# Performance work log

Measured on AMD Instinct MI355X. Metric: run time of the kernel, lower is better.

The kernel has to match this reference:

```python
import jax, jax.numpy as jnp
import numpy as np

B, S, I, H = 2, 400, 80, 128
F = 2 * H            # bidirectional feature dim
N = S + 1            # zero row prepended -> pairwise grid size
MAX_SEG = 50
NCLS = 50


def prelu(x, a):
    return jnp.where(x >= 0, x, a * x)


def lstm_dir(x, Wi, Wh, b, reverse=False):
    # x: (B, S, I); torch gate order: i, f, g, o
    if reverse:
        x = x[:, ::-1]
    Hd = Wh.shape[1]

    def step(carry, xt):
        h, c = carry
        gates = xt @ Wi.T + h @ Wh.T + b
        i_, f_, g_, o_ = jnp.split(gates, 4, axis=-1)
        c = jax.nn.sigmoid(f_) * c + jax.nn.sigmoid(i_) * jnp.tanh(g_)
        h = jax.nn.sigmoid(o_) * jnp.tanh(c)
        return (h, c), h

    h0 = jnp.zeros((x.shape[0], Hd), x.dtype)
    _, hs = jax.lax.scan(step, (h0, h0), jnp.swapaxes(x, 0, 1))
    hs = jnp.swapaxes(hs, 0, 1)
    if reverse:
        hs = hs[:, ::-1]
    return hs


def setup_inputs() -> dict:
    key = jax.random.key(0)
    ks = jax.random.split(key, 16)

    def rn(k, shape, s=0.05):
        return jax.random.normal(k, shape, jnp.float32) * s

    inp = {
        "x": jax.random.normal(ks[0], (B, S, I), jnp.float32),
        "lengths": jnp.full((B,), S, jnp.int32),
        "Wi_f": rn(ks[1], (4 * H, I)), "Wh_f": rn(ks[2], (4 * H, H)), "b_f": jnp.zeros((4 * H,), jnp.float32),
        "Wi_b": rn(ks[3], (4 * H, I)), "Wh_b": rn(ks[4], (4 * H, H)), "b_b": jnp.zeros((4 * H,), jnp.float32),
        "a1": jnp.full((1,), 0.25, jnp.float32),
        "W1": rn(ks[5], (100, 3 * F)), "b1": jnp.zeros((100,), jnp.float32),
        "a2": jnp.full((1,), 0.25, jnp.float32),
        "W2": rn(ks[6], (1, 100)), "b2": jnp.zeros((1,), jnp.float32),
        "ac1": jnp.full((1,), 0.25, jnp.float32),
        "Wc1": rn(ks[7], (2 * NCLS, F)), "bc1": jnp.zeros((2 * NCLS,), jnp.float32),
        "ac2": jnp.full((1,), 0.25, jnp.float32),
        "Wc2": rn(ks[8], (NCLS, 2 * NCLS)), "bc2": jnp.zeros((NCLS,), jnp.float32),
        "ab1": jnp.full((1,), 0.25, jnp.float32),
        "Wb1": rn(ks[9], (2 * NCLS, F)), "bb1": jnp.zeros((2 * NCLS,), jnp.float32),
        "ab2": jnp.full((1,), 0.25, jnp.float32),
        "Wb2": rn(ks[10], (2, 2 * NCLS)), "bb2": jnp.zeros((2,), jnp.float32),
    }
    return inp


def compute_scores(x, Wi_f, Wh_f, b_f, Wi_b, Wh_b, b_b, a1, W1, b1, a2, W2, b2):
    rnn_out = jnp.concatenate(
        [lstm_dir(x, Wi_f, Wh_f, b_f, False), lstm_dir(x, Wi_b, Wh_b, b_b, True)], axis=-1
    )  # (B, S, F)
    xp = jnp.concatenate([jnp.zeros((x.shape[0], 1, F), x.dtype), rnn_out], axis=1)  # (B, N, F)
    cum = jnp.cumsum(xp, axis=1)
    # phi[b,i,j] = concat(cum[j]-cum[i], xp[i], xp[j]); PReLU is elementwise with a
    # single shared parameter, and the first Linear is additive across the concat
    # blocks, so we decompose W1 instead of materializing the (B,N,N,3F) tensor.
    W1c, W1d, W1e = W1[:, :F], W1[:, F:2 * F], W1[:, 2 * F:]
    pc = prelu(cum[:, None, :, :] - cum[:, :, None, :], a1)  # (B, N, N, F)
    pxd = prelu(xp, a1) @ W1d.T                              # (B, N, 100)
    pxe = prelu(xp, a1) @ W1e.T                              # (B, N, 100)
    h = jnp.einsum('bijf,kf->bijk', pc, W1c) + pxd[:, :, None, :] + pxe[:, None, :, :] + b1
    scores = (prelu(h, a2) @ W2.T + b2)[..., 0]              # (B, N, N)
    return rnn_out, scores


def segment_search(scores):
    # DP: best[i] = max_{max(0,i-MAX_SEG) <= k < i} best[k] + scores[:, k, i]
    Bn, Nn = scores.shape[0], scores.shape[1]
    ks = jnp.arange(Nn)

    def dp_step(best, i):
        col = jnp.take(scores, i, axis=2)                    # (B, N)
        mask = (ks >= i - MAX_SEG) & (ks < i)
        cand = jnp.where(mask[None, :], best + col, -jnp.inf)
        m = cand.max(axis=1)
        k = cand.argmax(axis=1)
        best = best.at[:, i].set(m)
        return best, k

    best0 = jnp.zeros((Bn, Nn), scores.dtype)
    best, prev_tail = jax.lax.scan(dp_step, best0, jnp.arange(1, Nn))
    prev = jnp.concatenate([jnp.zeros((Bn, 1), jnp.int32),
                            prev_tail.T.astype(jnp.int32)], axis=1)  # (B, N)
    return best, prev


def reference(x, lengths, Wi_f, Wh_f, b_f, Wi_b, Wh_b, b_b, a1, W1, b1, a2, W2, b2,
              ac1, Wc1, bc1, ac2, Wc2, bc2, ab1, Wb1, bb1, ab2, Wb2, bb2):
    rnn_out, scores = compute_scores(x, Wi_f, Wh_f, b_f, Wi_b, Wh_b, b_b,
                                     a1, W1, b1, a2, W2, b2)
    cls_out = prelu(prelu(rnn_out, ac1) @ Wc1.T + bc1, ac2) @ Wc2.T + bc2
    bin_out = prelu(prelu(rnn_out, ab1) @ Wb1.T + bb1, ab2) @ Wb2.T + bb2
    best, prev = segment_search(scores)
    # pred score for the best segmentation ending at `lengths[b]` equals best[b, L]
    pred_scores = best[jnp.arange(scores.shape[0]), lengths]
    return scores, cls_out, bin_out, pred_scores, prev
```

## Files before the change

### kernel.cpp

```cpp
#include <hip/hip_runtime.h>
#include <hip/hip_fp16.h>
#include <math.h>

#define BB 2
#define SS 400
#define II 80
#define HH 128
#define FF 256
#define NN 401
#define G4 512
#define MAXSEG 50
#define NCLS 50
#define KH 100
#define KP 112
#define FRAGF 14336

#define SCORES_OFF 0
#define CLS_OFF    (BB*NN*NN)
#define BIN_OFF    (CLS_OFF + BB*SS*NCLS)
#define PRED_OFF   (BIN_OFF + BB*SS*2)
#define PREV_OFF   (PRED_OFF + BB)

#define WS_GX      0
#define WS_RNN     (WS_GX + 4*SS*G4)
#define WS_CUM     (WS_RNN + BB*SS*FF)
#define WS_PXD     (WS_CUM + BB*NN*FF)
#define WS_PXE     (WS_PXD + BB*NN*KP)
#define WS_PART    (WS_PXE + BB*NN*KP)
#define WS_W2P     (WS_PART + BB*16*FF)
#define WS_B1P     (WS_W2P + KP)
#define WS_WHP     (WS_B1P + KP)
#define WS_WFRAGC  (WS_WHP + 65536)
#define WS_WFRAGD  (WS_WFRAGC + FRAGF)
#define WS_WFRAGE  (WS_WFRAGD + FRAGF)
#define WS_WFRAGHC (WS_WFRAGE + FRAGF)
#define WS_WFRAGHB (WS_WFRAGHC + FRAGF)
#define WS_BC1P    (WS_WFRAGHB + FRAGF)
#define WS_BB1P    (WS_BC1P + KP)

typedef __attribute__((ext_vector_type(8))) short short8;
typedef __attribute__((ext_vector_type(4))) float f32x4;
typedef _Float16 f16x2 __attribute__((ext_vector_type(2)));
typedef _Float16 f16x8 __attribute__((ext_vector_type(8)));

__device__ __forceinline__ float prelu_f(float x, float a) {
    return x >= 0.f ? x : a * x;
}
__device__ __forceinline__ unsigned short f2bf(float x) {
    union { float f; unsigned u; } v; v.f = x;
    unsigned r = v.u + 0x7fffu + ((v.u >> 16) & 1u);
    return (unsigned short)(r >> 16);
}
__device__ __forceinline__ float fast_sigmoid(float x) {
    return 1.f / (1.f + __expf(-x));
}
__device__ __forceinline__ float fast_tanh(float x) {
    return 1.f - 2.f / (1.f + __expf(2.f * x));
}
__device__ __forceinline__ void barrier_lds() {
    asm volatile("s_waitcnt lgkmcnt(0)\ns_barrier" ::: "memory");
}
__device__ __forceinline__ void rec_barrier() {
    __builtin_amdgcn_sched_barrier(0);
    asm volatile("s_waitcnt lgkmcnt(0)");
    __builtin_amdgcn_s_barrier();
    __builtin_amdgcn_sched_barrier(0);
}
__device__ __forceinline__ int fragidx(int k, int f) {
    int kt = k >> 4, l15 = k & 15;
    int ks = f >> 5, quad = (f >> 3) & 3, e = f & 7;
    return ((((kt * 8 + ks) * 4 + quad) * 16) + l15) * 8 + e;
}

#define WPACKS (5 * KP)
#define PREPBLKS (WPACKS + G4)
__global__ void k_lstm_pre(const float* __restrict__ x,
                           const float* __restrict__ Wi_f, const float* __restrict__ b_f,
                           const float* __restrict__ Wi_b, const float* __restrict__ b_b,
                           float* __restrict__ gx,
                           const float* __restrict__ W1, const float* __restrict__ W2,
                           const float* __restrict__ b1,
                           const float* __restrict__ Wh_f, const float* __restrict__ Wh_b,
                           const float* __restrict__ Wc1, const float* __restrict__ Wb1,
                           const float* __restrict__ bc1, const float* __restrict__ bb1,
                           short* __restrict__ wfC, short* __restrict__ wfD,
                           short* __restrict__ wfE, short* __restrict__ wfHC,
                           short* __restrict__ wfHB,
                           float* __restrict__ w2p, float* __restrict__ b1p,
                           float* __restrict__ bc1p, float* __restrict__ bb1p,
                           __half* __restrict__ whp) {
    int blk0 = blockIdx.x;
    int tid = threadIdx.x;
    if (blk0 < WPACKS) {
        int which = blk0 / KP;
        int k = blk0 % KP;
        float w = 0.f;
        short* dst = wfC;
        if (which == 0)      { if (k < KH) w = W1[k * (3 * FF) + tid];          dst = wfC; }
        else if (which == 1) { if (k < KH) w = W1[k * (3 * FF) + FF + tid];     dst = wfD; }
        else if (which == 2) { if (k < KH) w = W1[k * (3 * FF) + 2 * FF + tid]; dst = wfE; }
        else if (which == 3) { if (k < KH) w = Wc1[k * FF + tid];               dst = wfHC; }
        else                 { if (k < KH) w = Wb1[k * FF + tid];               dst = wfHB; }
        dst[fragidx(k, tid)] = (short)f2bf(w);
        if (tid == 0) {
            if (which == 0) {
                w2p[k] = (k < KH) ? W2[k] : 0.f;
                b1p[k] = (k < KH) ? b1[k] : 0.f;
            } else if (which == 3) {
                bc1p[k] = (k < KH) ? bc1[k] : 0.f;
            } else if (which == 4) {
                bb1p[k] = (k < KH) ? bb1[k] : 0.f;
            }
        }
        return;
    }
    if (blk0 < PREPBLKS) {
        int gq = blk0 - WPACKS;
        int gate = gq >> 7;
        int unit = gq & 127;
        int wv = unit >> 4, col = unit & 15;
        int dir = tid >> 7, k = tid & 127;
        int kt = k >> 5, lanehi = (k >> 3) & 3, e = k & 7;
        int lane = lanehi * 16 + col;
        const float* Wh = dir ? Wh_b : Wh_f;
        whp[(size_t)(((((dir * 4 + gate) * 8 + wv) * 4 + kt) * 64) + lane) * 8 + e] =
            (__half)Wh[gq * HH + k];
        return;
    }
    int blk = blk0 - PREPBLKS;
    int t = blk % SS;
    int db = blk / SS;
    int b = db & 1, dir = db >> 1;
    const float* Wi = dir ? Wi_b : Wi_f;
    const float* bias = dir ? b_b : b_f;
    int xt = dir ? (SS - 1 - t) : t;

    __shared__ __align__(16) float xr[II];
    if (tid < II) xr[tid] = x[(b * SS + xt) * II + tid];
    __syncthreads();

    for (int g = tid; g < G4; g += 256) {
        const float* w = Wi + g * II;
        float acc = bias[g];
#pragma unroll
        for (int i = 0; i < II; i += 4) {
            float4 w4 = *(const float4*)(w + i);
            acc += w4.x * xr[i] + w4.y * xr[i + 1] + w4.z * xr[i + 2] + w4.w * xr[i + 3];
        }
        gx[((size_t)(db * SS + t) * HH + (g & 127)) * 4 + (g >> 7)] = acc;
    }
}

__global__ __launch_bounds__(512, 1)
void k_lstm_rec(const _Float16* __restrict__ whf, const float* __restrict__ gxr,
                float* __restrict__ rnn_out) {
    int db = blockIdx.x;
    int b = db & 1, dir = db >> 1;
    int tid = threadIdx.x;
    int wv = tid >> 6;
    int lane = tid & 63;

    f16x8 bf[4][4];
    {
        const f16x8* wp = (const f16x8*)whf;
#pragma unroll
        for (int g = 0; g < 4; ++g)
#pragma unroll
            for (int kt = 0; kt < 4; ++kt)
                bf[g][kt] = wp[((((dir * 4 + g) * 8 + wv) * 4 + kt) * 64) + lane];
    }

    __shared__ __align__(16) __half hsf[2][128];
    for (int i = tid; i < 256; i += 512) (&hsf[0][0])[i] = (__half)0.f;
    __syncthreads();

    float c_state = 0.f;
    const float4* gp4 = (const float4*)gxr + (size_t)(db * SS) * HH
                      + (wv << 4) + (lane & 15);

    float4 g0 = make_float4(0,0,0,0), g1 = g0, g2 = g0, g3 = g0;
    if (lane < 16) {
        g0 = gp4[0 * HH];
        g1 = gp4[1 * HH];
        g2 = gp4[2 * HH];
        g3 = gp4[3 * HH];
    }
    const float4* gq = gp4 + (size_t)4 * HH;

    float* outp = rnn_out + ((size_t)b * SS + (dir ? (SS - 1) : 0)) * FF
                + dir * HH + (wv << 4) + lane;
    const int ostep = dir ? -FF : FF;

    const f32x4 z4 = (f32x4){0.f, 0.f, 0.f, 0.f};
    int pb = 0;
    int hib = (lane >> 4) * 8;

#define REC_STEP(G, PF) do {                                                   \
        f16x8 a0 = *(const f16x8*)(&hsf[pb][ 0 + hib]);                        \
        f16x8 a1 = *(const f16x8*)(&hsf[pb][32 + hib]);                        \
        f16x8 a2 = *(const f16x8*)(&hsf[pb][64 + hib]);                        \
        f16x8 a3 = *(const f16x8*)(&hsf[pb][96 + hib]);                        \
        f32x4 acc0 = __builtin_amdgcn_mfma_f32_16x16x32_f16(a0, bf[0][0], z4, 0, 0, 0); \
        f32x4 acc1 = __builtin_amdgcn_mfma_f32_16x16x32_f16(a0, bf[1][0], z4, 0, 0, 0); \
        f32x4 acc2 = __builtin_amdgcn_mfma_f32_16x16x32_f16(a0, bf[2][0], z4, 0, 0, 0); \
        f32x4 acc3 = __builtin_amdgcn_mfma_f32_16x16x32_f16(a0, bf[3][0], z4, 0, 0, 0); \
        acc0 = __builtin_amdgcn_mfma_f32_16x16x32_f16(a1, bf[0][1], acc0, 0, 0, 0); \
        acc1 = __builtin_amdgcn_mfma_f32_16x16x32_f16(a1, bf[1][1], acc1, 0, 0, 0); \
        acc2 = __builtin_amdgcn_mfma_f32_16x16x32_f16(a1, bf[2][1], acc2, 0, 0, 0); \
        acc3 = __builtin_amdgcn_mfma_f32_16x16x32_f16(a1, bf[3][1], acc3, 0, 0, 0); \
        acc0 = __builtin_amdgcn_mfma_f32_16x16x32_f16(a2, bf[0][2], acc0, 0, 0, 0); \
        acc1 = __builtin_amdgcn_mfma_f32_16x16x32_f16(a2, bf[1][2], acc1, 0, 0, 0); \
        acc2 = __builtin_amdgcn_mfma_f32_16x16x32_f16(a2, bf[2][2], acc2, 0, 0, 0); \
        acc3 = __builtin_amdgcn_mfma_f32_16x16x32_f16(a2, bf[3][2], acc3, 0, 0, 0); \
        acc0 = __builtin_amdgcn_mfma_f32_16x16x32_f16(a3, bf[0][3], acc0, 0, 0, 0); \
        acc1 = __builtin_amdgcn_mfma_f32_16x16x32_f16(a3, bf[1][3], acc1, 0, 0, 0); \
        acc2 = __builtin_amdgcn_mfma_f32_16x16x32_f16(a3, bf[2][3], acc2, 0, 0, 0); \
        acc3 = __builtin_amdgcn_mfma_f32_16x16x32_f16(a3, bf[3][3], acc3, 0, 0, 0); \
        if (lane < 16) {                                                       \
            float gi = acc0[0] + G.x;                                          \
            float gf = acc1[0] + G.y;                                          \
            float gg = acc2[0] + G.z;                                          \
            float go = acc3[0] + G.w;                                          \
            if (PF) { G = *gq; gq += HH; }         \
            c_state = fast_sigmoid(gf) * c_state + fast_sigmoid(gi) * fast_tanh(gg); \
            float h = fast_sigmoid(go) * fast_tanh(c_state);                   \
            hsf[pb ^ 1][(wv << 4) + lane] = (__half)h;                         \
            *outp = h;                                                         \
            outp += ostep;                                                     \
        }                                                                      \
        rec_barrier();                                                         \
        pb ^= 1;                                                               \
    } while (0)

    for (int it = 0; it < 99; ++it) {
        REC_STEP(g0, 1);
        REC_STEP(g1, 1);
        REC_STEP(g2, 1);
        REC_STEP(g3, 1);
    }
    REC_STEP(g0, 0);
    REC_STEP(g1, 0);
    REC_STEP(g2, 0);
    REC_STEP(g3, 0);
#undef REC_STEP
}

__global__ void k_cum(const float* __restrict__ rnn, float* __restrict__ cum) {
    int b = blockIdx.x;
    int f = threadIdx.x;
    float run = 0.f;
    cum[(size_t)(b * NN) * FF + f] = 0.f;
    const float* rp = rnn + (size_t)b * SS * FF + f;
    float* cp = cum + ((size_t)b * NN + 1) * FF + f;
#pragma unroll 8
    for (int t = 0; t < SS; ++t) {
        run += rp[(size_t)t * FF];
        cp[(size_t)t * FF] = run;
    }
}

#define PXBLKS 26
#define HDBLKS 25
#define AP 272
#define UCP 116
__global__ __launch_bounds__(256, 2)
void k_mlp(const float* __restrict__ rnn,
           const float* __restrict__ a1p,
           const float* __restrict__ ac1p, const float* __restrict__ ab1p,
           const short* __restrict__ wfD, const short* __restrict__ wfE,
           const short* __restrict__ wfHC, const short* __restrict__ wfHB,
           const float* __restrict__ bc1p, const float* __restrict__ bb1p,
           const float* __restrict__ ac2p, const float* __restrict__ ab2p,
           const float* __restrict__ Wc2, const float* __restrict__ bc2,
           const float* __restrict__ Wb2, const float* __restrict__ bb2,
           float* __restrict__ pxd, float* __restrict__ pxe,
           float* __restrict__ cls_out, float* __restrict__ bin_out) {
    int blk = blockIdx.x;
    int tid = threadIdx.x;
    bool is_px = (blk < PXBLKS);
    int rowbase = is_px ? blk * 32 : (blk - PXBLKS) * 32;
    int nrows_tot = is_px ? BB * NN : BB * SS;

    __shared__ __align__(16) short dth[2][32][AP];
    __shared__ float ucsh[2][32][UCP];

    {
        int row = tid >> 3;
        int fb = (tid & 7) * 32;
        int rg = rowbase + row;
        float src[32];
        if (is_px) {
            float a1 = a1p[0];
            int b = rg / NN, n = rg % NN;
            bool valid = (rg < nrows_tot) && (n > 0);
            const float* sp = valid ? (rnn + (b * SS + n - 1) * FF + fb) : nullptr;
#pragma unroll
            for (int c4 = 0; c4 < 8; ++c4) {
                float4 v = valid ? *(const float4*)(sp + c4 * 4) : make_float4(0,0,0,0);
                src[c4*4] = v.x; src[c4*4+1] = v.y; src[c4*4+2] = v.z; src[c4*4+3] = v.w;
            }
            union { short8 s; unsigned short u[8]; } h8;
#pragma unroll
            for (int c8 = 0; c8 < 4; ++c8) {
#pragma unroll
                for (int e = 0; e < 8; ++e) h8.u[e] = f2bf(prelu_f(src[c8*8+e], a1));
                *(short8*)(&dth[0][row][fb + c8 * 8]) = h8.s;
            }
        } else {
            float ac1 = ac1p[0], ab1 = ab1p[0];
            bool valid = (rg < nrows_tot);
            const float* sp = valid ? (rnn + rg * FF + fb) : nullptr;
#pragma unroll
            for (int c4 = 0; c4 < 8; ++c4) {
                float4 v = valid ? *(const float4*)(sp + c4 * 4) : make_float4(0,0,0,0);
                src[c4*4] = v.x; src[c4*4+1] = v.y; src[c4*4+2] = v.z; src[c4*4+3] = v.w;
            }
            union { short8 s; unsigned short u[8]; } hc, hb;
#pragma unroll
            for (int c8 = 0; c8 < 4; ++c8) {
#pragma unroll
                for (int e = 0; e < 8; ++e) {
                    hc.u[e] = f2bf(prelu_f(src[c8*8+e], ac1));
                    hb.u[e] = f2bf(prelu_f(src[c8*8+e], ab1));
                }
                *(short8*)(&dth[0][row][fb + c8 * 8]) = hc.s;
                *(short8*)(&dth[1][row][fb + c8 * 8]) = hb.s;
            }
        }
    }
    __syncthreads();

    int lane = tid & 63;
    int wv = tid >> 6;
    int quad = lane >> 4;
    int l15 = lane & 15;
    int kt0 = wv * 2, kt1 = wv * 2 + 1;
    bool has1 = (kt1 < 7);

    const short8* wp0 = (const short8*)(is_px ? wfD : wfHC);
    const short8* wp1 = (const short8*)(is_px ? wfE : wfHB);

    f32x4 acc[2][2][2];
#pragma unroll
    for (int p = 0; p < 2; ++p)
#pragma unroll
        for (int mt = 0; mt < 2; ++mt)
#pragma unroll
            for (int kk = 0; kk < 2; ++kk) acc[p][mt][kk] = (f32x4){0.f,0.f,0.f,0.f};

#pragma unroll
    for (int ks = 0; ks < 8; ++ks) {
        short8 b00 = wp0[((kt0 * 8 + ks) * 4 + quad) * 16 + l15];
        short8 b01 = has1 ? wp0[((kt1 * 8 + ks) * 4 + quad) * 16 + l15] : b00;
        short8 b10 = wp1[((kt0 * 8 + ks) * 4 + quad) * 16 + l15];
        short8 b11 = has1 ? wp1[((kt1 * 8 + ks) * 4 + quad) * 16 + l15] : b10;
#pragma unroll
        for (int mt = 0; mt < 2; ++mt) {
            short8 a0 = *(const short8*)(&dth[0][mt * 16 + l15][ks * 32 + quad * 8]);
            short8 a1v = is_px ? a0
                       : *(const short8*)(&dth[1][mt * 16 + l15][ks * 32 + quad * 8]);
            acc[0][mt][0] = __builtin_amdgcn_mfma_f32_16x16x32_bf16(a0, b00, acc[0][mt][0], 0, 0, 0);
            acc[1][mt][0] = __builtin_amdgcn_mfma_f32_16x16x32_bf16(a1v, b10, acc[1][mt][0], 0, 0, 0);
            if (has1) {
                acc[0][mt][1] = __builtin_amdgcn_mfma_f32_16x16x32_bf16(a0, b01, acc[0][mt][1], 0, 0, 0);
                acc[1][mt][1] = __builtin_amdgcn_mfma_f32_16x16x32_bf16(a1v, b11, acc[1][mt][1], 0, 0, 0);
            }
        }
    }

    int kout0 = kt0 * 16 + l15;
    int kout1 = has1 ? (kt1 * 16 + l15) : 0;

    if (is_px) {
#pragma unroll
        for (int mt = 0; mt < 2; ++mt) {
#pragma unroll
            for (int r = 0; r < 4; ++r) {
                int m = mt * 16 + quad * 4 + r;
                int rg = rowbase + m;
                if (rg < nrows_tot) {
                    pxd[rg * KP + kout0] = acc[0][mt][0][r];
                    pxe[rg * KP + kout0] = acc[1][mt][0][r];
                    if (has1) {
                        pxd[rg * KP + kout1] = acc[0][mt][1][r];
                        pxe[rg * KP + kout1] = acc[1][mt][1][r];
                    }
                }
            }
        }
        return;
    }

    float bc0 = bc1p[kout0], bc1v = bc1p[kout1];
    float bb0 = bb1p[kout0], bb1v = bb1p[kout1];
    float ac2 = ac2p[0], ab2 = ab2p[0];
#pragma unroll
    for (int mt = 0; mt < 2; ++mt) {
#pragma unroll
        for (int r = 0; r < 4; ++r) {
            int m = mt * 16 + quad * 4 + r;
            ucsh[0][m][kout0] = prelu_f(acc[0][mt][0][r] + bc0, ac2);
            ucsh[1][m][kout0] = prelu_f(acc[1][mt][0][r] + bb0, ab2);
            if (has1) {
                ucsh[0][m][kout1] = prelu_f(acc[0][mt][1][r] + bc1v, ac2);
                ucsh[1][m][kout1] = prelu_f(acc[1][mt][1][r] + bb1v, ab2);
            }
        }
    }
    __syncthreads();
    {
        int row = tid >> 3;
        int oc = tid & 7;
        int rg = rowbase + row;
        bool valid = (rg < nrows_tot);
        for (int o = oc; o < NCLS; o += 8) {
            float s = bc2[o];
            const float* w = Wc2 + o * KH;
#pragma unroll 4
            for (int k = 0; k < KH; ++k) s += w[k] * ucsh[0][row][k];
            if (valid) cls_out[rg * NCLS + o] = s;
        }
        if (tid < 64) {
            int row2 = tid >> 1, o = tid & 1;
            int rg2 = rowbase + row2;
            float s = bb2[o];
            const float* w = Wb2 + o * KH;
#pragma unroll 4
            for (int k = 0; k < KH; ++k) s += w[k] * ucsh[1][row2][k];
            if (rg2 < nrows_tot) bin_out[rg2 * 2 + o] = s;
        }
    }
}

#define JT 32
#define JTILES 13
#define NP2 201
__global__ __launch_bounds__(256, 3)
void k_scores(const float* __restrict__ cum,
              const short* __restrict__ wfrag,
              const float* __restrict__ pxd, const float* __restrict__ pxe,
              const float* __restrict__ b1p, const float* __restrict__ w2p,
              const float* __restrict__ b2p,
              const float* __restrict__ a1p, const float* __restrict__ a2p,
              float* __restrict__ scores, float* __restrict__ dpcol) {
    int blk = blockIdx.x;
    int jt = blk % JTILES;
    int ipair = (blk / JTILES) % NP2;
    int b = blk / (JTILES * NP2);
    int tid = threadIdx.x;
    float a1 = a1p[0], a2 = a2p[0];
    int jbase = jt * JT;
    int i0 = ipair * 2;
    int i1 = i0 + 1;
    bool has_i1 = (i1 <= SS);
    int i1c = has_i1 ? i1 : i0;

    __shared__ __align__(16) float cish[2][FF];
    __shared__ __align__(16) short dth[2][JT][AP];
    __shared__ float red[2][4][JT];

    cish[0][tid] = cum[(b * NN + i0) * FF + tid];
    cish[1][tid] = cum[(b * NN + i1c) * FF + tid];
    __syncthreads();

    {
        int row = tid >> 3;
        int fb = (tid & 7) * 32;
        int jg = jbase + row;
        int jc = (jg <= SS) ? jg : SS;
        const float* cj = cum + (b * NN + jc) * FF + fb;
        float4 v[8];
#pragma unroll
        for (int c8 = 0; c8 < 4; ++c8) {
            v[2 * c8] = *(const float4*)(cj + c8 * 8);
            v[2 * c8 + 1] = *(const float4*)(cj + c8 * 8 + 4);
        }
#pragma unroll
        for (int ii = 0; ii < 2; ++ii) {
            const float* cio = &cish[ii][0];
#pragma unroll
            for (int c8 = 0; c8 < 4; ++c8) {
                float dv[8] = { v[2*c8].x, v[2*c8].y, v[2*c8].z, v[2*c8].w,
                                v[2*c8+1].x, v[2*c8+1].y, v[2*c8+1].z, v[2*c8+1].w };
                union { short8 s; unsigned short u[8]; } h8;
#pragma unroll
                for (int e = 0; e < 8; ++e) {
                    float d = prelu_f(dv[e] - cio[fb + c8 * 8 + e], a1);
                    h8.u[e] = f2bf(d);
                }
                *(short8*)(&dth[ii][row][fb + c8 * 8]) = h8.s;
            }
        }
    }
    __syncthreads();

    int lane = tid & 63;
    int wv = tid >> 6;
    int quad = lane >> 4;
    int l15 = lane & 15;
    int kt0 = wv * 2, kt1 = wv * 2 + 1;
    bool has1 = (kt1 < 7);

    const short8* wf = (const short8*)wfrag;
    f32x4 acc[2][2][2];
#pragma unroll
    for (int ii = 0; ii < 2; ++ii)
#pragma unroll
        for (int mt = 0; mt < 2; ++mt)
#pragma unroll
            for (int kk = 0; kk < 2; ++kk) acc[ii][mt][kk] = (f32x4){0.f,0.f,0.f,0.f};

#pragma unroll
    for (int ks = 0; ks < 8; ++ks) {
        short8 b0 = wf[((kt0 * 8 + ks) * 4 + quad) * 16 + l15];
        short8 b1v = has1 ? wf[((kt1 * 8 + ks) * 4 + quad) * 16 + l15] : b0;
#pragma unroll
        for (int ii = 0; ii < 2; ++ii) {
#pragma unroll
            for (int mt = 0; mt < 2; ++mt) {
                short8 a = *(const short8*)(&dth[ii][mt * 16 + l15][ks * 32 + quad * 8]);
                acc[ii][mt][0] = __builtin_amdgcn_mfma_f32_16x16x32_bf16(a, b0, acc[ii][mt][0], 0, 0, 0);
                if (has1)
                    acc[ii][mt][1] = __builtin_amdgcn_mfma_f32_16x16x32_bf16(a, b1v, acc[ii][mt][1], 0, 0, 0);
            }
        }
    }

    int kout0 = kt0 * 16 + l15;
    int kout1 = has1 ? (kt1 * 16 + l15) : 0;
    float bb0 = b1p[kout0], bb1v = b1p[kout1];
    float w20 = w2p[kout0];
    float w21 = has1 ? w2p[kout1] : 0.f;

#pragma unroll
    for (int ii = 0; ii < 2; ++ii) {
        int iv = ii ? i1c : i0;
        float pd0 = pxd[(b * NN + iv) * KP + kout0];
        float pd1 = pxd[(b * NN + iv) * KP + kout1];
#pragma unroll
        for (int mt = 0; mt < 2; ++mt) {
#pragma unroll
            for (int r = 0; r < 4; ++r) {
                int m = mt * 16 + quad * 4 + r;
                int jg = jbase + m;
                int jc = (jg <= SS) ? jg : SS;
                float pe0 = pxe[(b * NN + jc) * KP + kout0];
                float pe1 = pxe[(b * NN + jc) * KP + kout1];
                float h0 = acc[ii][mt][0][r] + pd0 + pe0 + bb0;
                float s = w20 * prelu_f(h0, a2);
                float h1 = acc[ii][mt][1][r] + pd1 + pe1 + bb1v;
                s += w21 * prelu_f(h1, a2);
                s += __shfl_xor(s, 1);
                s += __shfl_xor(s, 2);
                s += __shfl_xor(s, 4);
                s += __shfl_xor(s, 8);
                if (l15 == 0) red[ii][wv][m] = s;
            }
        }
    }
    __syncthreads();
    if (tid < 2 * JT) {
        int ii = tid >> 5;
        int jl = tid & 31;
        int jg = jbase + jl;
        int iv = ii ? i1 : i0;
        if (jg <= SS && (ii == 0 || has_i1)) {
            float tot = red[ii][0][jl] + red[ii][1][jl] + red[ii][2][jl] + red[ii][3][jl] + b2p[0];
            scores[(b * NN + iv) * NN + jg] = tot;
            int d = jg - iv;
            if (d >= 1 && d <= MAXSEG) {
                dpcol[(b * NN + jg) * 64 + (iv & 63)] = tot;
            }
        }
    }
}

__global__ void k_dp(const float* __restrict__ dpcol, const int* __restrict__ lengths,
                     float* __restrict__ predF, float* __restrict__ prevF) {
    int b = blockIdx.x;
    int lane = threadIdx.x;
    int len = lengths[b];
    if (lane == 0) prevF[b * NN] = 0.f;

    float blr = 0.f;
    float predv = 0.f;

#define LO(I) (((I) > MAXSEG) ? ((I) - MAXSEG) : 0)
#define LOADCOL(ii) \
    ( ((ii) <= SS && (((lane - LO(ii)) & 63) < ((ii) - LO(ii)))) \
        ? dpcol[(b * NN + (ii)) * 64 + lane] : 0.f )

    float u0 = LOADCOL(1), u1 = LOADCOL(2), u2 = LOADCOL(3), u3 = LOADCOL(4);
    float u4 = LOADCOL(5), u5 = LOADCOL(6), u6 = LOADCOL(7), u7 = LOADCOL(8);

#define DPP_LVL(CTRL, v, k) do {                                              \
        int vo_i = __builtin_amdgcn_update_dpp(__float_as_int(v),             \
                       __float_as_int(v), (CTRL), 0xF, 0xF, false);           \
        int ko_  = __builtin_amdgcn_update_dpp((k), (k), (CTRL), 0xF, 0xF, false); \
        float vo = __int_as_float(vo_i);                                      \
        bool take = (vo > (v)) || (vo == (v) && ko_ < (k));                   \
        (v) = take ? vo : (v);                                                \
        (k) = take ? ko_ : (k);                                               \
    } while (0)

#define DP_STEP(I, BUF) do {                                                  \
        int lo_ = LO(I);                                                      \
        int cnt_ = (I) - lo_;                                                 \
        int off_ = (lane - lo_) & 63;                                         \
        float v_ = (off_ < cnt_) ? blr + BUF : -INFINITY;                     \
        int k_ = lo_ + off_;                                                  \
        DPP_LVL(0x111, v_, k_);                               \
        DPP_LVL(0x112, v_, k_);                               \
        DPP_LVL(0x114, v_, k_);                               \
        DPP_LVL(0x118, v_, k_);                               \
        DPP_LVL(0x142, v_, k_);                             \
        DPP_LVL(0x143, v_, k_);                             \
        int kb_ = __builtin_amdgcn_readlane(k_, 63);                          \
        float m_ = __int_as_float(                                            \
            __builtin_amdgcn_readlane(__float_as_int(v_), 63));               \
        if (lane == 0) {                                                      \
            prevF[b * NN + (I)] = (float)kb_;                                 \
            if ((I) == len) predv = m_;                                       \
        }                                                                     \
        if (lane == ((I) & 63)) blr = m_;                                     \
    } while (0)

    for (int i = 1; i <= SS; i += 8) {
        DP_STEP(i, u0);     u0 = LOADCOL(i + 8);
        DP_STEP(i + 1, u1); u1 = LOADCOL(i + 9);
        DP_STEP(i + 2, u2); u2 = LOADCOL(i + 10);
        DP_STEP(i + 3, u3); u3 = LOADCOL(i + 11);
        DP_STEP(i + 4, u4); u4 = LOADCOL(i + 12);
        DP_STEP(i + 5, u5); u5 = LOADCOL(i + 13);
        DP_STEP(i + 6, u6); u6 = LOADCOL(i + 14);
        DP_STEP(i + 7, u7); u7 = LOADCOL(i + 15);
    }
#undef DP_STEP
#undef DPP_LVL
#undef LOADCOL
#undef LO
    if (lane == 0) predF[b] = predv;
}

extern "C" void kernel_launch(void* const* d_in, const int* in_sizes, int n_in,
                              void* d_out, int out_size, void* d_ws, size_t ws_size,
                              hipStream_t stream) {
    const float* x    = (const float*)d_in[0];
    const int* lengths= (const int*)d_in[1];
    const float* Wi_f = (const float*)d_in[2];
    const float* Wh_f = (const float*)d_in[3];
    const float* b_f  = (const float*)d_in[4];
    const float* Wi_b = (const float*)d_in[5];
    const float* Wh_b = (const float*)d_in[6];
    const float* b_b  = (const float*)d_in[7];
    const float* a1   = (const float*)d_in[8];
    const float* W1   = (const float*)d_in[9];
    const float* b1   = (const float*)d_in[10];
    const float* a2   = (const float*)d_in[11];
    const float* W2   = (const float*)d_in[12];
    const float* b2   = (const float*)d_in[13];
    const float* ac1  = (const float*)d_in[14];
    const float* Wc1  = (const float*)d_in[15];
    const float* bc1  = (const float*)d_in[16];
    const float* ac2  = (const float*)d_in[17];
    const float* Wc2  = (const float*)d_in[18];
    const float* bc2  = (const float*)d_in[19];
    const float* ab1  = (const float*)d_in[20];
    const float* Wb1  = (const float*)d_in[21];
    const float* bb1  = (const float*)d_in[22];
    const float* ab2  = (const float*)d_in[23];
    const float* Wb2  = (const float*)d_in[24];
    const float* bb2  = (const float*)d_in[25];

    float* out = (float*)d_out;
    float* scores = out + SCORES_OFF;
    float* cls    = out + CLS_OFF;
    float* bin    = out + BIN_OFF;
    float* pred   = out + PRED_OFF;
    float* prev   = out + PREV_OFF;

    float* ws    = (float*)d_ws;
    float* gx    = ws + WS_GX;
    float* dpcol = ws + WS_GX;
    float* rnn   = ws + WS_RNN;
    float* cum   = ws + WS_CUM;
    float* pxd   = ws + WS_PXD;
    float* pxe   = ws + WS_PXE;
    float* w2p   = ws + WS_W2P;
    float* b1p   = ws + WS_B1P;
    __half* whp  = (__half*)(ws + WS_WHP);
    short* wfC   = (short*)(ws + WS_WFRAGC);
    short* wfD   = (short*)(ws + WS_WFRAGD);
    short* wfE   = (short*)(ws + WS_WFRAGE);
    short* wfHC  = (short*)(ws + WS_WFRAGHC);
    short* wfHB  = (short*)(ws + WS_WFRAGHB);
    float* bc1p  = ws + WS_BC1P;
    float* bb1p  = ws + WS_BB1P;

    k_lstm_pre<<<PREPBLKS + 4 * SS, 256, 0, stream>>>(x, Wi_f, b_f, Wi_b, b_b, gx,
                                                      W1, W2, b1, Wh_f, Wh_b,
                                                      Wc1, Wb1, bc1, bb1,
                                                      wfC, wfD, wfE, wfHC, wfHB,
                                                      w2p, b1p, bc1p, bb1p, whp);
    k_lstm_rec<<<4, 512, 0, stream>>>((const _Float16*)whp, gx, rnn);
    k_cum<<<BB, FF, 0, stream>>>(rnn, cum);
    k_mlp<<<PXBLKS + HDBLKS, 256, 0, stream>>>(rnn, a1, ac1, ab1,
                                               wfD, wfE, wfHC, wfHB,
                                               bc1p, bb1p, ac2, ab2,
                                               Wc2, bc2, Wb2, bb2,
                                               pxd, pxe, cls, bin);
    k_scores<<<BB * NP2 * JTILES, 256, 0, stream>>>(cum, wfC, pxd, pxe, b1p, w2p, b2,
                                                    a1, a2, scores, dpcol);
    k_dp<<<BB, 64, 0, stream>>>(dpcol, lengths, pred, prev);
}
```

Before: 648.7 us.

## Halve LSTM recurrence block to 4 waves, each computing two hidden-unit tiles

The recurrent LSTM kernel now runs with 256 threads (4 waves) instead of 512. Each wave holds two sets of weight fragments and issues 32 MFMAs per step to cover 32 hidden units. The aim is to make the per-timestep block barrier cheaper, since fewer waves have to synchronise on every one of the 400 serial steps. In exchange each wave has twice the MFMA work on the critical path and more register pressure. The A-operand LDS load is also restricted to every fourth lane, relying on MFMA only reading those lanes' data.

```diff
diff --git a/kernel.cpp b/kernel.cpp
--- a/kernel.cpp
+++ b/kernel.cpp
@@ -151,7 +151,7 @@
     }
 }
 
-__global__ __launch_bounds__(512, 1)
+__global__ __launch_bounds__(256, 1)
 void k_lstm_rec(const _Float16* __restrict__ whf, const float* __restrict__ gxr,
                 float* __restrict__ rnn_out) {
     int db = blockIdx.x;
@@ -160,26 +160,30 @@
     int wv = tid >> 6;
     int lane = tid & 63;
 
-    f16x8 bf[4][4];
+    f16x8 bfA[4][4], bfB[4][4];
     {
         const f16x8* wp = (const f16x8*)whf;
 #pragma unroll
         for (int g = 0; g < 4; ++g)
 #pragma unroll
-            for (int kt = 0; kt < 4; ++kt)
-                bf[g][kt] = wp[((((dir * 4 + g) * 8 + wv) * 4 + kt) * 64) + lane];
+            for (int kt = 0; kt < 4; ++kt) {
+                bfA[g][kt] = wp[((((dir * 4 + g) * 8 + (2 * wv)) * 4 + kt) * 64) + lane];
+                bfB[g][kt] = wp[((((dir * 4 + g) * 8 + (2 * wv + 1)) * 4 + kt) * 64) + lane];
+            }
     }
 
     __shared__ __align__(16) __half hsf[2][128];
-    for (int i = tid; i < 256; i += 512) (&hsf[0][0])[i] = (__half)0.f;
+    (&hsf[0][0])[tid] = (__half)0.f;
     __syncthreads();
 
+    bool act = (lane < 32);
+    bool grpB = (lane >= 16);
+    int unit = (wv << 5) + (lane & 31);
     float c_state = 0.f;
-    const float4* gp4 = (const float4*)gxr + (size_t)(db * SS) * HH
-                      + (wv << 4) + (lane & 15);
-
+
+    const float4* gp4 = (const float4*)gxr + (size_t)(db * SS) * HH + unit;
     float4 g0 = make_float4(0,0,0,0), g1 = g0, g2 = g0, g3 = g0;
-    if (lane < 16) {
+    if (act) {
         g0 = gp4[0 * HH];
         g1 = gp4[1 * HH];
         g2 = gp4[2 * HH];
@@ -188,43 +192,64 @@
     const float4* gq = gp4 + (size_t)4 * HH;
 
     float* outp = rnn_out + ((size_t)b * SS + (dir ? (SS - 1) : 0)) * FF
-                + dir * HH + (wv << 4) + lane;
+                + dir * HH + unit;
     const int ostep = dir ? -FF : FF;
 
     const f32x4 z4 = (f32x4){0.f, 0.f, 0.f, 0.f};
     int pb = 0;
     int hib = (lane >> 4) * 8;
+    bool aload = (lane & 3) == 0;
+
+    f16x8 a0v = (f16x8)(_Float16)0.f, a1v = a0v, a2v = a0v, a3v = a0v;
 
 #define REC_STEP(G, PF) do {                                                   \
-        f16x8 a0 = *(const f16x8*)(&hsf[pb][ 0 + hib]);                        \
-        f16x8 a1 = *(const f16x8*)(&hsf[pb][32 + hib]);                        \
-        f16x8 a2 = *(const f16x8*)(&hsf[pb][64 + hib]);                        \
-        f16x8 a3 = *(const f16x8*)(&hsf[pb][96 + hib]);                        \
-        f32x4 acc0 = __builtin_amdgcn_mfma_f32_16x16x32_f16(a0, bf[0][0], z4, 0, 0, 0); \
-        f32x4 acc1 = __builtin_amdgcn_mfma_f32_16x16x32_f16(a0, bf[1][0], z4, 0, 0, 0); \
-        f32x4 acc2 = __builtin_amdgcn_mfma_f32_16x16x32_f16(a0, bf[2][0], z4, 0, 0, 0); \
-        f32x4 acc3 = __builtin_amdgcn_mfma_f32_16x16x32_f16(a0, bf[3][0], z4, 0, 0, 0); \
-        acc0 = __builtin_amdgcn_mfma_f32_16x16x32_f16(a1, bf[0][1], acc0, 0, 0, 0); \
-        acc1 = __builtin_amdgcn_mfma_f32_16x16x32_f16(a1, bf[1][1], acc1, 0, 0, 0); \
-        acc2 = __builtin_amdgcn_mfma_f32_16x16x32_f16(a1, bf[2][1], acc2, 0, 0, 0); \
-        acc3 = __builtin_amdgcn_mfma_f32_16x16x32_f16(a1, bf[3][1], acc3, 0, 0, 0); \
-        acc0 = __builtin_amdgcn_mfma_f32_16x16x32_f16(a2, bf[0][2], acc0, 0, 0, 0); \
-        acc1 = __builtin_amdgcn_mfma_f32_16x16x32_f16(a2, bf[1][2], acc1, 0, 0, 0); \
-        acc2 = __builtin_amdgcn_mfma_f32_16x16x32_f16(a2, bf[2][2], acc2, 0, 0, 0); \
-        acc3 = __builtin_amdgcn_mfma_f32_16x16x32_f16(a2, bf[3][2], acc3, 0, 0, 0); \
-        acc0 = __builtin_amdgcn_mfma_f32_16x16x32_f16(a3, bf[0][3], acc0, 0, 0, 0); \
-        acc1 = __builtin_amdgcn_mfma_f32_16x16x32_f16(a3, bf[1][3], acc1, 0, 0, 0); \
-        acc2 = __builtin_amdgcn_mfma_f32_16x16x32_f16(a3, bf[2][3], acc2, 0, 0, 0); \
-        acc3 = __builtin_amdgcn_mfma_f32_16x16x32_f16(a3, bf[3][3], acc3, 0, 0, 0); \
-        if (lane < 16) {                                                       \
-            float gi = acc0[0] + G.x;                                          \
-            float gf = acc1[0] + G.y;                                          \
-            float gg = acc2[0] + G.z;                                          \
-            float go = acc3[0] + G.w;                                          \
+        if (aload) {                                                           \
+            a0v = *(const f16x8*)(&hsf[pb][ 0 + hib]);                         \
+            a1v = *(const f16x8*)(&hsf[pb][32 + hib]);                         \
+            a2v = *(const f16x8*)(&hsf[pb][64 + hib]);                         \
+            a3v = *(const f16x8*)(&hsf[pb][96 + hib]);                         \
+        }                                                                      \
+        f32x4 aA0 = __builtin_amdgcn_mfma_f32_16x16x32_f16(a0v, bfA[0][0], z4, 0, 0, 0); \
+        f32x4 aA1 = __builtin_amdgcn_mfma_f32_16x16x32_f16(a0v, bfA[1][0], z4, 0, 0, 0); \
+        f32x4 aA2 = __builtin_amdgcn_mfma_f32_16x16x32_f16(a0v, bfA[2][0], z4, 0, 0, 0); \
+        f32x4 aA3 = __builtin_amdgcn_mfma_f32_16x16x32_f16(a0v, bfA[3][0], z4, 0, 0, 0); \
+        f32x4 aB0 = __builtin_amdgcn_mfma_f32_16x16x32_f16(a0v, bfB[0][0], z4, 0, 0, 0); \
+        f32x4 aB1 = __builtin_amdgcn_mfma_f32_16x16x32_f16(a0v, bfB[1][0], z4, 0, 0, 0); \
+        f32x4 aB2 = __builtin_amdgcn_mfma_f32_16x16x32_f16(a0v, bfB[2][0], z4, 0, 0, 0); \
+        f32x4 aB3 = __builtin_amdgcn_mfma_f32_16x16x32_f16(a0v, bfB[3][0], z4, 0, 0, 0); \
+        aA0 = __builtin_amdgcn_mfma_f32_16x16x32_f16(a1v, bfA[0][1], aA0, 0, 0, 0); \
+        aA1 = __builtin_amdgcn_mfma_f32_16x16x32_f16(a1v, bfA[1][1], aA1, 0, 0, 0); \
+        aA2 = __builtin_amdgcn_mfma_f32_16x16x32_f16(a1v, bfA[2][1], aA2, 0, 0, 0); \
+        aA3 = __builtin_amdgcn_mfma_f32_16x16x32_f16(a1v, bfA[3][1], aA3, 0, 0, 0); \
+        aB0 = __builtin_amdgcn_mfma_f32_16x16x32_f16(a1v, bfB[0][1], aB0, 0, 0, 0); \
+        aB1 = __builtin_amdgcn_mfma_f32_16x16x32_f16(a1v, bfB[1][1], aB1, 0, 0, 0); \
+        aB2 = __builtin_amdgcn_mfma_f32_16x16x32_f16(a1v, bfB[2][1], aB2, 0, 0, 0); \
+        aB3 = __builtin_amdgcn_mfma_f32_16x16x32_f16(a1v, bfB[3][1], aB3, 0, 0, 0); \
+        aA0 = __builtin_amdgcn_mfma_f32_16x16x32_f16(a2v, bfA[0][2], aA0, 0, 0, 0); \
+        aA1 = __builtin_amdgcn_mfma_f32_16x16x32_f16(a2v, bfA[1][2], aA1, 0, 0, 0); \
+        aA2 = __builtin_amdgcn_mfma_f32_16x16x32_f16(a2v, bfA[2][2], aA2, 0, 0, 0); \
+        aA3 = __builtin_amdgcn_mfma_f32_16x16x32_f16(a2v, bfA[3][2], aA3, 0, 0, 0); \
+        aB0 = __builtin_amdgcn_mfma_f32_16x16x32_f16(a2v, bfB[0][2], aB0, 0, 0, 0); \
+        aB1 = __builtin_amdgcn_mfma_f32_16x16x32_f16(a2v, bfB[1][2], aB1, 0, 0, 0); \
+        aB2 = __builtin_amdgcn_mfma_f32_16x16x32_f16(a2v, bfB[2][2], aB2, 0, 0, 0); \
+        aB3 = __builtin_amdgcn_mfma_f32_16x16x32_f16(a2v, bfB[3][2], aB3, 0, 0, 0); \
+        aA0 = __builtin_amdgcn_mfma_f32_16x16x32_f16(a3v, bfA[0][3], aA0, 0, 0, 0); \
+        aA1 = __builtin_amdgcn_mfma_f32_16x16x32_f16(a3v, bfA[1][3], aA1, 0, 0, 0); \
+        aA2 = __builtin_amdgcn_mfma_f32_16x16x32_f16(a3v, bfA[2][3], aA2, 0, 0, 0); \
+        aA3 = __builtin_amdgcn_mfma_f32_16x16x32_f16(a3v, bfA[3][3], aA3, 0, 0, 0); \
+        aB0 = __builtin_amdgcn_mfma_f32_16x16x32_f16(a3v, bfB[0][3], aB0, 0, 0, 0); \
+        aB1 = __builtin_amdgcn_mfma_f32_16x16x32_f16(a3v, bfB[1][3], aB1, 0, 0, 0); \
+        aB2 = __builtin_amdgcn_mfma_f32_16x16x32_f16(a3v, bfB[2][3], aB2, 0, 0, 0); \
+        aB3 = __builtin_amdgcn_mfma_f32_16x16x32_f16(a3v, bfB[3][3], aB3, 0, 0, 0); \
+        if (act) {                                                             \
+            float gi = (grpB ? aB0[0] : aA0[0]) + G.x;                         \
+            float gf = (grpB ? aB1[0] : aA1[0]) + G.y;                         \
+            float gg = (grpB ? aB2[0] : aA2[0]) + G.z;                         \
+            float go = (grpB ? aB3[0] : aA3[0]) + G.w;                         \
             if (PF) { G = *gq; gq += HH; }         \
             c_state = fast_sigmoid(gf) * c_state + fast_sigmoid(gi) * fast_tanh(gg); \
             float h = fast_sigmoid(go) * fast_tanh(c_state);                   \
-            hsf[pb ^ 1][(wv << 4) + lane] = (__half)h;                         \
+            hsf[pb ^ 1][unit] = (__half)h;                                     \
             *outp = h;                                                         \
             outp += ostep;                                                     \
         }                                                                      \
@@ -702,7 +727,7 @@
                                                       Wc1, Wb1, bc1, bb1,
                                                       wfC, wfD, wfE, wfHC, wfHB,
                                                       w2p, b1p, bc1p, bb1p, whp);
-    k_lstm_rec<<<4, 512, 0, stream>>>((const _Float16*)whp, gx, rnn);
+    k_lstm_rec<<<4, 256, 0, stream>>>((const _Float16*)whp, gx, rnn);
     k_cum<<<BB, FF, 0, stream>>>(rnn, cum);
     k_mlp<<<PXBLKS + HDBLKS, 256, 0, stream>>>(rnn, a1, ac1, ab1,
                                                wfD, wfE, wfHC, wfHB,
```

New measurement: 633.4 us. 2.4% less time.
